# Performance work log

Measured on AMD Instinct MI355X. Metric: run time of the kernel, lower is better.

Reference implementation:

```python
import jax, jax.numpy as jnp
import numpy as np
from jax import lax

# NOTE: ResidualConvBlock and SS2DChanelFirst are reconstructed from the repo's
# conventions: ResidualConvBlock = act(conv3x3 -> act -> conv3x3 + 1x1 skip);
# SS2DChanelFirst = standard VMamba SS2D (in_proj -> dw-conv3x3 -> SiLU ->
# 4-direction cross-scan selective scan -> cross-merge -> LayerNorm -> *SiLU(z)
# gate -> out_proj) operating on NCHW tensors.

B, CIN, H, W = 4, 6, 64, 64
DM, DI, K, N, R, NL, GROUPS = 72, 144, 4, 8, 4, 2, 12


def conv2d(x, w, b=None, groups=1):
    out = lax.conv_general_dilated(x, w, (1, 1), 'SAME',
                                   dimension_numbers=('NCHW', 'OIHW', 'NCHW'),
                                   feature_group_count=groups)
    if b is not None:
        out = out + b[None, :, None, None]
    return out


def lrelu(x, s):
    return jnp.where(x >= 0, x, s * x)


def selective_scan(u, delta, A, Bs, Cs, D):
    # u, delta: (b,K,C,L); A: (K,C,N); Bs, Cs: (b,K,N,L); D: (K,C)
    b, k, c, l = u.shape
    n = A.shape[-1]
    ul = jnp.moveaxis(u, -1, 0)
    dl = jnp.moveaxis(delta, -1, 0)
    Bl = jnp.moveaxis(Bs, -1, 0)
    Cl = jnp.moveaxis(Cs, -1, 0)
    h0 = jnp.zeros((b, k, c, n), u.dtype)

    def step(h, xt):
        d_t, u_t, B_t, C_t = xt
        h = h * jnp.exp(d_t[..., None] * A) + (d_t * u_t)[..., None] * B_t[:, :, None, :]
        return h, jnp.einsum('bkcn,bkn->bkc', h, C_t)

    _, ys = lax.scan(step, h0, (dl, ul, Bl, Cl))
    return jnp.moveaxis(ys, 0, -1) + u * D[None, :, :, None]


def ss2d(x, in_w, dw_w, dw_b, xp_w, dtp_w, dtp_b, A_logs, Ds, ong, onb, op_w):
    b, dm, h_, w_ = x.shape
    l = h_ * w_
    xz = jnp.einsum('ec,bchw->behw', in_w, x)  # (b, 2*DI, h, w)
    xi, z = xz[:, :DI], xz[:, DI:]
    xi = jax.nn.silu(conv2d(xi, dw_w, dw_b, groups=DI))
    # cross-scan: row-major, col-major, and their reverses
    x0 = xi.reshape(b, DI, l)
    x1 = jnp.swapaxes(xi, 2, 3).reshape(b, DI, l)
    xs = jnp.stack([x0, x1, x0[..., ::-1], x1[..., ::-1]], axis=1)  # (b,4,DI,l)
    x_dbl = jnp.einsum('bkdl,kcd->bkcl', xs, xp_w)  # (b,4,R+2N,l)
    dts, Bs, Cs = x_dbl[:, :, :R], x_dbl[:, :, R:R + N], x_dbl[:, :, R + N:]
    dts = jnp.einsum('bkrl,kdr->bkdl', dts, dtp_w)
    delta = jax.nn.softplus(dts + dtp_b[None, :, :, None])
    A = -jnp.exp(A_logs).reshape(K, DI, N)
    ys = selective_scan(xs, delta, A, Bs, Cs, Ds.reshape(K, DI))  # (b,4,DI,l)
    # cross-merge
    y = ys[:, 0] + ys[:, 2, :, ::-1]
    yt = ys[:, 1] + ys[:, 3, :, ::-1]
    y = y + jnp.swapaxes(yt.reshape(b, DI, w_, h_), 2, 3).reshape(b, DI, l)
    y = jnp.swapaxes(y, 1, 2)  # (b,l,DI)
    mu = y.mean(-1, keepdims=True)
    var = ((y - mu) ** 2).mean(-1, keepdims=True)
    y = (y - mu) / jnp.sqrt(var + 1e-5) * ong + onb
    y = y * jax.nn.silu(jnp.swapaxes(z.reshape(b, DI, l), 1, 2))
    out = jnp.einsum('bld,ed->ble', y, op_w)  # (b,l,DM)
    return jnp.swapaxes(out, 1, 2).reshape(b, dm, h_, w_)


def groupnorm(x, g, bta, groups):
    b, c, h_, w_ = x.shape
    xg = x.reshape(b, groups, c // groups, h_ * w_)
    mu = xg.mean((2, 3), keepdims=True)
    var = ((xg - mu) ** 2).mean((2, 3), keepdims=True)
    xg = (xg - mu) / jnp.sqrt(var + 1e-5)
    return xg.reshape(b, c, h_, w_) * g[None, :, None, None] + bta[None, :, None, None]


def setup_inputs() -> dict:
    key = jax.random.key(0)
    ks = iter(jax.random.split(key, 32))
    nrm = lambda shp, s=0.05: jax.random.normal(next(ks), shp, jnp.float32) * s
    inp = {
        'image': jax.random.normal(next(ks), (B, CIN, H, W), jnp.float32),
        'cb_w1': nrm((DM, CIN, 3, 3), 0.1), 'cb_b1': nrm((DM,), 0.02),
        'cb_w2': nrm((DM, DM, 3, 3), 0.05), 'cb_b2': nrm((DM,), 0.02),
        'cb_ws': nrm((DM, CIN, 1, 1), 0.1), 'cb_bs': nrm((DM,), 0.02),
        'in_w': nrm((NL, 2 * DI, DM), 0.05),
        'dw_w': nrm((NL, DI, 1, 3, 3), 0.1), 'dw_b': nrm((NL, DI), 0.02),
        'xp_w': nrm((NL, K, R + 2 * N, DI), 0.05),
        'dtp_w': nrm((NL, K, DI, R), 0.1), 'dtp_b': nrm((NL, K, DI), 0.1),
        'A_logs': nrm((NL, K * DI, N), 0.5),
        'Ds': jnp.ones((NL, K * DI), jnp.float32) + nrm((NL, K * DI), 0.05),
        'ong': jnp.ones((NL, DI), jnp.float32), 'onb': jnp.zeros((NL, DI), jnp.float32),
        'op_w': nrm((NL, DM, DI), 0.05),
        'gn_g': jnp.ones((NL, DM), jnp.float32), 'gn_b': jnp.zeros((NL, DM), jnp.float32),
        'l1_w': nrm((NL, DM, DM), 0.1), 'l1_b': nrm((NL, DM), 0.02),
        'l2_w': nrm((NL, DM, DM), 0.1), 'l2_b': nrm((NL, DM), 0.02),
        'shrink_w': nrm((CIN, DM, 3, 3), 0.05), 'shrink_b': nrm((CIN,), 0.02),
    }
    return inp


def reference(image, cb_w1, cb_b1, cb_w2, cb_b2, cb_ws, cb_bs, in_w, dw_w, dw_b,
              xp_w, dtp_w, dtp_b, A_logs, Ds, ong, onb, op_w, gn_g, gn_b,
              l1_w, l1_b, l2_w, l2_b, shrink_w, shrink_b):
    # ResidualConvBlock (expand 6 -> 72), leaky_relu
    h = lrelu(conv2d(image, cb_w1, cb_b1), 0.01)
    h = conv2d(h, cb_w2, cb_b2) + conv2d(image, cb_ws, cb_bs)
    x = lrelu(h, 0.01)
    for i in range(NL):
        x = ss2d(x, in_w[i], dw_w[i], dw_b[i], xp_w[i], dtp_w[i], dtp_b[i],
                 A_logs[i], Ds[i], ong[i], onb[i], op_w[i])
        x = groupnorm(x, gn_g[i], gn_b[i], GROUPS)
        x = jnp.einsum('oc,bchw->bohw', l1_w[i], x) + l1_b[i][None, :, None, None]
        x = lrelu(x, 0.04)
        x = jnp.einsum('oc,bchw->bohw', l2_w[i], x) + l2_b[i][None, :, None, None]
    x = conv2d(x, shrink_w, shrink_b)
    return jax.nn.sigmoid(x)
```

## Files before the change

### kernel.cpp

```cpp
#include <hip/hip_runtime.h>
#include <math.h>

#define BB 4
#define CI 6
#define LL 4096
#define DMC 72
#define DIC 144
#define KD 4
#define NS 8
#define RD 4
#define NLAYER 2
#define GRP 12
#define NCH 128
#define TS 32
#define PP 4356

__device__ __forceinline__ float sigmoidf_(float x){ return 1.f/(1.f+__expf(-x)); }
__device__ __forceinline__ float siluf_(float x){ return x*sigmoidf_(x); }
__device__ __forceinline__ float softplusf_(float x){
  return fmaxf(x,0.f) + __logf(1.f + __expf(-fabsf(x)));
}

__device__ __forceinline__ int padidx(int p){ return 66*(p>>6) + (p&63) + 67; }

__device__ __forceinline__ int dirmap(int k, int l){
  switch(k & 3){
    case 0: return l;
    case 1: return ((l & 63) << 6) | (l >> 6);
    case 2: return (LL-1) - l;
    default: { int m = (LL-1) - l; return ((m & 63) << 6) | (m >> 6); }
  }
}

#define LOAD9(ip, a) do { \
  a[0]=(ip)[-67]; a[1]=(ip)[-66]; a[2]=(ip)[-65]; \
  a[3]=(ip)[-1];  a[4]=(ip)[0];   a[5]=(ip)[1];   \
  a[6]=(ip)[65];  a[7]=(ip)[66];  a[8]=(ip)[67];  } while(0)

__global__ void k_halo(float* __restrict__ pads, int nplanes){
  int plane = blockIdx.x;
  if (plane >= nplanes) return;
  int t = threadIdx.x;
  if (t >= 260) return;
  float* pl = pads + (size_t)plane*PP;
  int off;
  if (t < 132){
    int row = (t < 66) ? 0 : 65;
    int col = (t < 66) ? t : t-66;
    off = row*66 + col;
  } else {
    int j = t - 132;
    int col = (j < 64) ? 0 : 65;
    int row = 1 + (j & 63);
    off = row*66 + col;
  }
  pl[off] = 0.f;
}

__global__ void k_pad_img(const float* __restrict__ img, float* __restrict__ img_pad){
  int idx = blockIdx.x*256 + threadIdx.x;
  if (idx >= BB*CI*LL) return;
  int p = idx & 4095; int bc = idx >> 12;
  img_pad[(size_t)bc*PP + padidx(p)] = img[idx];
}

__global__ void k_conv1(const float* __restrict__ img_pad, const float* __restrict__ w,
                        const float* __restrict__ bias, float* __restrict__ tmp_pad){
  int bid = blockIdx.x;
  int t = bid & 15; int r = bid >> 4; int o = r % DMC; int b = r / DMC;
  int p = t*256 + threadIdx.x;
  int pb = padidx(p);
  float acc = bias[o];
  const float* wb = w + o*CI*9;
  #pragma unroll
  for (int ic=0; ic<CI; ++ic){
    const float* ip = img_pad + (size_t)(b*CI+ic)*PP + pb;
    float a[9]; LOAD9(ip, a);
    #pragma unroll
    for (int q=0;q<9;++q) acc += a[q]*wb[ic*9+q];
  }
  tmp_pad[(size_t)(b*DMC+o)*PP + pb] = acc >= 0.f ? acc : 0.01f*acc;
}

__global__ void k_conv2(const float* __restrict__ tmp_pad, const float* __restrict__ img,
                        const float* __restrict__ w2, const float* __restrict__ b2,
                        const float* __restrict__ wsc, const float* __restrict__ bsc,
                        float* __restrict__ xout){
  int bid = blockIdx.x;
  int t = bid & 15; int r = bid >> 4; int og = r % 18; int b = r / 18;
  int p = t*256 + threadIdx.x;
  int pb = padidx(p);
  float acc[4];
  #pragma unroll
  for (int j=0;j<4;++j) acc[j] = b2[og*4+j] + bsc[og*4+j];
  const float* ipb = tmp_pad + (size_t)b*DMC*PP + pb;
  const float* wb  = w2 + (size_t)(og*4)*DMC*9;
  #pragma unroll 2
  for (int ic=0; ic<DMC; ++ic){
    const float* ip = ipb + (size_t)ic*PP;
    float a[9]; LOAD9(ip, a);
    const float* wp = wb + ic*9;
    #pragma unroll
    for (int j=0;j<4;++j){
      float s = 0.f;
      #pragma unroll
      for (int q=0;q<9;++q) s += a[q]*wp[(size_t)j*DMC*9 + q];
      acc[j] += s;
    }
  }
  #pragma unroll
  for (int ic=0; ic<CI; ++ic){
    float v = img[((b*CI+ic)<<12)+p];
    #pragma unroll
    for (int j=0;j<4;++j) acc[j] += v * wsc[(og*4+j)*CI+ic];
  }
  #pragma unroll
  for (int j=0;j<4;++j){
    float a = acc[j];
    xout[((b*DMC+og*4+j)<<12)+p] = a >= 0.f ? a : 0.01f*a;
  }
}

__global__ void k_xz(const float* __restrict__ x, const float* __restrict__ inw,
                     float* __restrict__ xz_pad, float* __restrict__ z_t){
  int bid = blockIdx.x;
  int t = bid & 15; int r = bid >> 4; int eg = r % 36; int b = r / 36;
  int p = t*256 + threadIdx.x;
  float acc[8] = {0.f,0.f,0.f,0.f,0.f,0.f,0.f,0.f};
  for (int c0=0; c0<DMC; c0+=4){
    float a[4];
    #pragma unroll
    for (int q=0;q<4;++q) a[q] = x[((b*DMC+c0+q)<<12)+p];
    #pragma unroll
    for (int j=0;j<8;++j){
      float4 w = *(const float4*)(inw + (eg*8+j)*DMC + c0);
      acc[j] += a[0]*w.x + a[1]*w.y + a[2]*w.z + a[3]*w.w;
    }
  }
  if (eg < 18){
    int pb = padidx(p);
    #pragma unroll
    for (int j=0;j<8;++j) xz_pad[(size_t)(b*DIC+eg*8+j)*PP + pb] = acc[j];
  } else {
    float* zb = z_t + ((size_t)b*LL+p)*DIC + (eg*8-DIC);
    *(float4*)(zb)   = make_float4(acc[0],acc[1],acc[2],acc[3]);
    *(float4*)(zb+4) = make_float4(acc[4],acc[5],acc[6],acc[7]);
  }
}

__global__ void k_dw(const float* __restrict__ xz_pad, const float* __restrict__ dww,
                     const float* __restrict__ dwb, float* __restrict__ xi_t){
  int bid = blockIdx.x;
  int t = bid & 15; int r = bid >> 4; int c = r % DIC; int b = r / DIC;
  int p = t*256 + threadIdx.x;
  int pb = padidx(p);
  const float* ip = xz_pad + (size_t)(b*DIC+c)*PP + pb;
  const float* wp = dww + c*9;
  float a[9]; LOAD9(ip, a);
  float acc = dwb[c];
  #pragma unroll
  for (int q=0;q<9;++q) acc += a[q]*wp[q];
  xi_t[((size_t)b*LL+p)*DIC + c] = siluf_(acc);
}

__global__ void k_xdbl(const float* __restrict__ xi_t, const float* __restrict__ xpw,
                       float* __restrict__ xdbl){
  int bid = blockIdx.x;
  int t = bid & 15; int r = bid >> 4;
  int kk = r & 3; r >>= 2; int part = r & 3; int b = r >> 2;
  int p = t*256 + threadIdx.x;
  const float* xib = xi_t + ((size_t)b*LL + p)*DIC;
  const float* wk = xpw + (size_t)(kk*20 + part*5)*DIC;
  float acc[5] = {0.f,0.f,0.f,0.f,0.f};
  for (int d=0; d<DIC; d+=4){
    float4 v = *(const float4*)(xib + d);
    #pragma unroll
    for (int c=0;c<5;++c){
      float4 w = *(const float4*)(wk + (size_t)c*DIC + d);
      acc[c] += v.x*w.x + v.y*w.y + v.z*w.z + v.w*w.w;
    }
  }
  float* dst = xdbl + ((size_t)(b*KD+kk)*LL + p)*20 + part*5;
  #pragma unroll
  for (int c=0;c<5;++c) dst[c] = acc[c];
}

__device__ __forceinline__ void scan_decode(int idx, int& b, int& k, int& ch, int& c){
  c = idx % DIC;
  int r = idx / DIC;
  ch = r % NCH;
  r /= NCH;
  k = r & 3; b = r >> 2;
}

__global__ void k_p1(const float* __restrict__ xi_t, const float* __restrict__ xdbl,
                     const float* __restrict__ dtpw, const float* __restrict__ dtpb,
                     const float* __restrict__ alog,
                     float* __restrict__ cumA, float* __restrict__ hp){
  int idx = blockIdx.x*256 + threadIdx.x;
  if (idx >= BB*KD*NCH*DIC) return;
  int b,k,ch,c; scan_decode(idx,b,k,ch,c);
  float Arow[NS];
  #pragma unroll
  for (int n=0;n<NS;++n) Arow[n] = -__expf(alog[(k*DIC+c)*NS+n]);
  float4 wdt = *(const float4*)(dtpw + (k*DIC+c)*RD);
  float bdt = dtpb[k*DIC+c];
  const float* xd = xdbl + (size_t)(b*KD+k)*LL*20;
  const float* xib = xi_t + (size_t)b*LL*DIC + c;
  float h[NS];
  #pragma unroll
  for (int n=0;n<NS;++n) h[n]=0.f;
  float sumd = 0.f;
  #pragma unroll 2
  for (int t=0; t<TS; ++t){
    int l = ch*TS + t;
    int ps = dirmap(k,l);
    const float* row = xd + (size_t)ps*20;
    float4 q0 = *(const float4*)(row);
    float4 q1 = *(const float4*)(row+4);
    float4 q2 = *(const float4*)(row+8);
    float u = xib[(size_t)ps*DIC];
    float dt = bdt + q0.x*wdt.x + q0.y*wdt.y + q0.z*wdt.z + q0.w*wdt.w;
    dt = softplusf_(dt);
    sumd += dt;
    float du = dt*u;
    float Bv[NS] = {q1.x,q1.y,q1.z,q1.w,q2.x,q2.y,q2.z,q2.w};
    #pragma unroll
    for (int n=0;n<NS;++n)
      h[n] = h[n]*__expf(dt*Arow[n]) + du*Bv[n];
  }
  size_t base = ((size_t)((b*KD+k)*NCH + ch)*NS)*DIC + c;
  #pragma unroll
  for (int n=0;n<NS;++n) hp[base + n*DIC] = h[n];
  #pragma unroll
  for (int n=0;n<NS;++n) cumA[base + n*DIC] = __expf(sumd*Arow[n]);
}

__global__ void k_p2(const float* __restrict__ cumA, float* __restrict__ hp){
  int idx = blockIdx.x*256 + threadIdx.x;
  if (idx >= BB*KD*NS*DIC) return;
  int c = idx % DIC; int n = (idx/DIC) % NS; int bk = idx/(DIC*NS);
  float h = 0.f;
  #pragma unroll 4
  for (int ch=0; ch<NCH; ++ch){
    size_t base = ((size_t)(bk*NCH+ch)*NS + n)*DIC + c;
    float a = cumA[base];
    float pp = hp[base];
    hp[base] = h;
    h = a*h + pp;
  }
}

__global__ void k_p3(const float* __restrict__ xi_t, const float* __restrict__ xdbl,
                     const float* __restrict__ dtpw, const float* __restrict__ dtpb,
                     const float* __restrict__ alog, const float* __restrict__ Dsv,
                     const float* __restrict__ hin, float* __restrict__ y_t){
  int idx = blockIdx.x*256 + threadIdx.x;
  if (idx >= BB*KD*NCH*DIC) return;
  int b,k,ch,c; scan_decode(idx,b,k,ch,c);
  float Arow[NS];
  #pragma unroll
  for (int n=0;n<NS;++n) Arow[n] = -__expf(alog[(k*DIC+c)*NS+n]);
  float4 wdt = *(const float4*)(dtpw + (k*DIC+c)*RD);
  float bdt = dtpb[k*DIC+c];
  float Dv = Dsv[k*DIC+c];
  const float* xd = xdbl + (size_t)(b*KD+k)*LL*20;
  const float* xib = xi_t + (size_t)b*LL*DIC + c;
  float* yb = y_t + (size_t)b*LL*DIC + c;
  float h[NS];
  size_t base = ((size_t)((b*KD+k)*NCH + ch)*NS)*DIC + c;
  #pragma unroll
  for (int n=0;n<NS;++n) h[n] = hin[base + n*DIC];
  #pragma unroll 2
  for (int t=0; t<TS; ++t){
    int l = ch*TS + t;
    int ps = dirmap(k,l);
    const float* row = xd + (size_t)ps*20;
    float4 q0 = *(const float4*)(row);
    float4 q1 = *(const float4*)(row+4);
    float4 q2 = *(const float4*)(row+8);
    float4 q3 = *(const float4*)(row+12);
    float4 q4 = *(const float4*)(row+16);
    float u = xib[(size_t)ps*DIC];
    float dt = bdt + q0.x*wdt.x + q0.y*wdt.y + q0.z*wdt.z + q0.w*wdt.w;
    dt = softplusf_(dt);
    float du = dt*u;
    float Bv[NS] = {q1.x,q1.y,q1.z,q1.w,q2.x,q2.y,q2.z,q2.w};
    float Cv[NS] = {q3.x,q3.y,q3.z,q3.w,q4.x,q4.y,q4.z,q4.w};
    float y = 0.f;
    #pragma unroll
    for (int n=0;n<NS;++n){
      h[n] = h[n]*__expf(dt*Arow[n]) + du*Bv[n];
      y += h[n]*Cv[n];
    }
    y += u*Dv;
    atomicAdd(yb + (size_t)ps*DIC, y);
  }
}

__global__ void k_oproj(const float* __restrict__ y_t, const float* __restrict__ z_t,
                        const float* __restrict__ ong, const float* __restrict__ onb,
                        const float* __restrict__ opw, float* __restrict__ xout){
  __shared__ float ly[DIC*65];
  __shared__ float red1[4][64], red2[4][64];
  __shared__ float lmu[64], lrs[64];
  int bid = blockIdx.x;
  int tile = bid & 63; int b = bid >> 6;
  int pstart = tile*64;
  const float* src = y_t + ((size_t)b*LL + pstart)*DIC;
  for (int i = threadIdx.x; i < 64*DIC; i += 256){
    int px = i / DIC; int d = i - px*DIC;
    ly[d*65 + px] = src[i];
  }
  __syncthreads();
  int px = threadIdx.x & 63;
  int grp = threadIdx.x >> 6;
  {
    float s=0.f, q=0.f;
    for (int d=grp*36; d<grp*36+36; ++d){
      float v = ly[d*65+px]; s += v; q += v*v;
    }
    red1[grp][px]=s; red2[grp][px]=q;
  }
  __syncthreads();
  if (grp == 0){
    float st = red1[0][px]+red1[1][px]+red1[2][px]+red1[3][px];
    float qt = red2[0][px]+red2[1][px]+red2[2][px]+red2[3][px];
    float mu = st*(1.f/DIC);
    float var = qt*(1.f/DIC) - mu*mu;
    lmu[px] = mu;
    lrs[px] = rsqrtf(var + 1e-5f);
  }
  __syncthreads();
  const float* zsrc = z_t + ((size_t)b*LL + pstart)*DIC;
  for (int i = threadIdx.x; i < 64*DIC; i += 256){
    int ppx = i / DIC; int d = i - ppx*DIC;
    float zv = zsrc[i];
    float v = ly[d*65+ppx];
    ly[d*65+ppx] = ((v - lmu[ppx])*lrs[ppx]*ong[d] + onb[d]) * siluf_(zv);
  }
  __syncthreads();
  int ocg = __builtin_amdgcn_readfirstlane(grp);
  float acc[18];
  #pragma unroll
  for (int j=0;j<18;++j) acc[j]=0.f;
  const float* wb = opw + (size_t)ocg*18*DIC;
  #pragma unroll 4
  for (int d=0; d<DIC; ++d){
    float a = ly[d*65 + px];
    #pragma unroll
    for (int j=0;j<18;++j) acc[j] += a * wb[(size_t)j*DIC + d];
  }
  #pragma unroll
  for (int j=0;j<18;++j)
    xout[((size_t)(b*DMC + ocg*18 + j)<<12) + pstart + px] = acc[j];
}

__global__ void k_gn(float* __restrict__ x, const float* __restrict__ g,
                     const float* __restrict__ bta){
  __shared__ float s1[256], s2[256];
  int b = blockIdx.x / GRP; int gr = blockIdx.x % GRP;
  const int CG = DMC/GRP;
  float ls=0.f, lq=0.f;
  for (int i = threadIdx.x; i < CG*LL; i += 256){
    int c = gr*CG + (i>>12); int p = i & 4095;
    float v = x[((size_t)(b*DMC+c)<<12)+p];
    ls += v; lq += v*v;
  }
  s1[threadIdx.x]=ls; s2[threadIdx.x]=lq; __syncthreads();
  for (int s=128; s>0; s>>=1){
    if (threadIdx.x < s){ s1[threadIdx.x]+=s1[threadIdx.x+s]; s2[threadIdx.x]+=s2[threadIdx.x+s]; }
    __syncthreads();
  }
  float mu = s1[0]/(CG*LL);
  float var = s2[0]/(CG*LL) - mu*mu;
  float rs = rsqrtf(var + 1e-5f);
  for (int i = threadIdx.x; i < CG*LL; i += 256){
    int c = gr*CG + (i>>12); int p = i & 4095;
    size_t off = ((size_t)(b*DMC+c)<<12)+p;
    x[off] = (x[off]-mu)*rs*g[c] + bta[c];
  }
}

__global__ void k_dense(const float* __restrict__ xin, const float* __restrict__ w,
                        const float* __restrict__ bias, float* __restrict__ xout,
                        float* __restrict__ pad_out, int do_lrelu){
  int bid = blockIdx.x;
  int t = bid & 15; int r = bid >> 4; int eg = r % 18; int b = r / 18;
  int p = t*256 + threadIdx.x;
  float acc[4];
  #pragma unroll
  for (int j=0;j<4;++j) acc[j] = bias[eg*4+j];
  for (int c0=0; c0<DMC; c0+=4){
    float a[4];
    #pragma unroll
    for (int q=0;q<4;++q) a[q] = xin[((size_t)(b*DMC+c0+q)<<12)+p];
    #pragma unroll
    for (int j=0;j<4;++j){
      float4 w0 = *(const float4*)(w + (eg*4+j)*DMC + c0);
      acc[j] += a[0]*w0.x + a[1]*w0.y + a[2]*w0.z + a[3]*w0.w;
    }
  }
  int pb = padidx(p);
  #pragma unroll
  for (int j=0;j<4;++j){
    float a = acc[j];
    if (do_lrelu) a = a >= 0.f ? a : 0.04f*a;
    xout[((size_t)(b*DMC+eg*4+j)<<12)+p] = a;
    if (pad_out) pad_out[(size_t)(b*DMC+eg*4+j)*PP + pb] = a;
  }
}

__global__ void k_shrinkA(const float* __restrict__ x_pad, const float* __restrict__ w,
                          float* __restrict__ pacc){
  int bid = blockIdx.x;
  int t = bid & 15; int r = bid >> 4; int icg = r & 7; int b = r >> 3;
  int p = t*256 + threadIdx.x;
  int pb = padidx(p);
  float acc[6] = {0.f,0.f,0.f,0.f,0.f,0.f};
  const float* ipb = x_pad + (size_t)b*DMC*PP + pb;
  #pragma unroll
  for (int ii=0; ii<9; ++ii){
    int ic = icg*9 + ii;
    const float* ip = ipb + (size_t)ic*PP;
    float a[9]; LOAD9(ip, a);
    #pragma unroll
    for (int o=0;o<6;++o){
      const float* wp = w + (o*DMC+ic)*9;
      float s = 0.f;
      #pragma unroll
      for (int q=0;q<9;++q) s += a[q]*wp[q];
      acc[o] += s;
    }
  }
  #pragma unroll
  for (int o=0;o<6;++o)
    atomicAdd(pacc + ((size_t)(b*CI+o)<<12)+p, acc[o]);
}

__global__ void k_sig(const float* __restrict__ pacc, const float* __restrict__ bias,
                      float* __restrict__ out){
  int idx = blockIdx.x*256 + threadIdx.x;
  if (idx >= BB*CI*LL) return;
  int o = (idx>>12) % CI;
  out[idx] = sigmoidf_(pacc[idx] + bias[o]);
}

extern "C" void kernel_launch(void* const* d_in, const int* in_sizes, int n_in,
                              void* d_out, int out_size, void* d_ws, size_t ws_size,
                              hipStream_t stream){
  const float* image = (const float*)d_in[0];
  const float* cb_w1 = (const float*)d_in[1];
  const float* cb_b1 = (const float*)d_in[2];
  const float* cb_w2 = (const float*)d_in[3];
  const float* cb_b2 = (const float*)d_in[4];
  const float* cb_ws = (const float*)d_in[5];
  const float* cb_bs = (const float*)d_in[6];
  const float* in_w  = (const float*)d_in[7];
  const float* dw_w  = (const float*)d_in[8];
  const float* dw_b  = (const float*)d_in[9];
  const float* xp_w  = (const float*)d_in[10];
  const float* dtp_w = (const float*)d_in[11];
  const float* dtp_b = (const float*)d_in[12];
  const float* A_logs= (const float*)d_in[13];
  const float* Ds    = (const float*)d_in[14];
  const float* ong   = (const float*)d_in[15];
  const float* onb   = (const float*)d_in[16];
  const float* op_w  = (const float*)d_in[17];
  const float* gn_g  = (const float*)d_in[18];
  const float* gn_b  = (const float*)d_in[19];
  const float* l1_w  = (const float*)d_in[20];
  const float* l1_b  = (const float*)d_in[21];
  const float* l2_w  = (const float*)d_in[22];
  const float* l2_b  = (const float*)d_in[23];
  const float* sh_w  = (const float*)d_in[24];
  const float* sh_b  = (const float*)d_in[25];

  const size_t SZ_X  = (size_t)BB*DMC*LL;
  const size_t SZ_C  = (size_t)BB*DIC*LL;
  const size_t SZ_XD = (size_t)BB*KD*20*LL;
  const size_t SZ_IP = (size_t)BB*CI*PP;
  const size_t SZ_TP = (size_t)BB*DMC*PP;
  const size_t SZ_ZP = (size_t)BB*DIC*PP;

  float* ws = (float*)d_ws;
  size_t off = 0;
  float* x     = ws + off; off += SZ_X;
  float* tmp   = ws + off; off += SZ_X;
  float* z_t   = ws + off; off += SZ_C;
  float* xi_t  = ws + off; off += SZ_C;
  float* xdbl  = ws + off; off += SZ_XD;
  float* cumA  = ws + off; off += SZ_C;
  float* hp    = ws + off; off += SZ_C;
  float* pads  = ws + off;
  float* img_pad = pads;
  float* tmp_pad = img_pad + SZ_IP;
  float* xz_pad  = tmp_pad + SZ_TP;
  off += SZ_IP + SZ_TP + SZ_ZP;
  if (ws_size < off*sizeof(float)) return;
  float* y_t = cumA;

  dim3 blk(256);
  const int NPLANES = BB*CI + BB*DMC + BB*DIC;

  k_halo<<<dim3(NPLANES), blk, 0, stream>>>(pads, NPLANES);
  k_pad_img<<<dim3(BB*CI*16), blk, 0, stream>>>(image, img_pad);
  k_conv1<<<dim3(BB*DMC*16), blk, 0, stream>>>(img_pad, cb_w1, cb_b1, tmp_pad);
  k_conv2<<<dim3(BB*18*16), blk, 0, stream>>>(tmp_pad, image, cb_w2, cb_b2, cb_ws, cb_bs, x);

  for (int i=0; i<NLAYER; ++i){
    const float* in_w_i  = in_w  + (size_t)i*2*DIC*DMC;
    const float* dw_w_i  = dw_w  + (size_t)i*DIC*9;
    const float* dw_b_i  = dw_b  + (size_t)i*DIC;
    const float* xp_w_i  = xp_w  + (size_t)i*KD*20*DIC;
    const float* dtp_w_i = dtp_w + (size_t)i*KD*DIC*RD;
    const float* dtp_b_i = dtp_b + (size_t)i*KD*DIC;
    const float* alog_i  = A_logs+ (size_t)i*KD*DIC*NS;
    const float* Ds_i    = Ds    + (size_t)i*KD*DIC;
    const float* ong_i   = ong   + (size_t)i*DIC;
    const float* onb_i   = onb   + (size_t)i*DIC;
    const float* op_w_i  = op_w  + (size_t)i*DMC*DIC;
    const float* gn_g_i  = gn_g  + (size_t)i*DMC;
    const float* gn_b_i  = gn_b  + (size_t)i*DMC;
    const float* l1_w_i  = l1_w  + (size_t)i*DMC*DMC;
    const float* l1_b_i  = l1_b  + (size_t)i*DMC;
    const float* l2_w_i  = l2_w  + (size_t)i*DMC*DMC;
    const float* l2_b_i  = l2_b  + (size_t)i*DMC;

    k_xz  <<<dim3(BB*36*16), blk, 0, stream>>>(x, in_w_i, xz_pad, z_t);
    k_dw  <<<dim3(BB*DIC*16), blk, 0, stream>>>(xz_pad, dw_w_i, dw_b_i, xi_t);
    k_xdbl<<<dim3(BB*KD*KD*16), blk, 0, stream>>>(xi_t, xp_w_i, xdbl);
    k_p1  <<<dim3(BB*KD*NCH*DIC/256), blk, 0, stream>>>(xi_t, xdbl, dtp_w_i, dtp_b_i, alog_i, cumA, hp);
    k_p2  <<<dim3(BB*KD*NS*DIC/256), blk, 0, stream>>>(cumA, hp);
    hipMemsetAsync(y_t, 0, SZ_C*sizeof(float), stream);
    k_p3  <<<dim3(BB*KD*NCH*DIC/256), blk, 0, stream>>>(xi_t, xdbl, dtp_w_i, dtp_b_i, alog_i, Ds_i, hp, y_t);
    k_oproj<<<dim3(BB*64), blk, 0, stream>>>(y_t, z_t, ong_i, onb_i, op_w_i, x);
    k_gn  <<<dim3(BB*GRP), blk, 0, stream>>>(x, gn_g_i, gn_b_i);
    k_dense<<<dim3(BB*18*16), blk, 0, stream>>>(x, l1_w_i, l1_b_i, tmp, (float*)nullptr, 1);
    k_dense<<<dim3(BB*18*16), blk, 0, stream>>>(tmp, l2_w_i, l2_b_i, x,
                                                (i==NLAYER-1) ? tmp_pad : (float*)nullptr, 0);
  }

  hipMemsetAsync(tmp, 0, (size_t)BB*CI*LL*sizeof(float), stream);
  k_shrinkA<<<dim3(BB*8*16), blk, 0, stream>>>(tmp_pad, sh_w, tmp);
  k_sig<<<dim3((BB*CI*LL+255)/256), blk, 0, stream>>>(tmp, sh_b, (float*)d_out);
}
```

Before: 528.2 us.

## Split kernels for more parallelism, parallelize groupnorm, and use exp2 in scan

Splits conv2 across two input-channel halves and accumulates with atomics, after a separate init kernel writes the skip path and bias. The leaky ReLU moves into the first in-projection load. Groupnorm becomes a parallel stats pass plus a per-channel scale/shift that is folded into the first dense layer, and the second dense layer applies the previous leaky ReLU on load. xdbl, dense and shrink kernels get finer output splits, oproj uses 512 threads, and the scan uses exp2f with a pre-scaled A. The goal is higher occupancy on small grids, removing the serialized 48-block groupnorm and cheaper exponentials, at the cost of extra launches and atomic traffic.

```diff
diff --git a/kernel.cpp b/kernel.cpp
--- a/kernel.cpp
+++ b/kernel.cpp
@@ -14,6 +14,7 @@
 #define NCH 128
 #define TS 32
 #define PP 4356
+#define L2E 1.4426950408889634f
 
 __device__ __forceinline__ float sigmoidf_(float x){ return 1.f/(1.f+__expf(-x)); }
 __device__ __forceinline__ float siluf_(float x){ return x*sigmoidf_(x); }
@@ -82,21 +83,39 @@
   tmp_pad[(size_t)(b*DMC+o)*PP + pb] = acc >= 0.f ? acc : 0.01f*acc;
 }
 
-__global__ void k_conv2(const float* __restrict__ tmp_pad, const float* __restrict__ img,
-                        const float* __restrict__ w2, const float* __restrict__ b2,
-                        const float* __restrict__ wsc, const float* __restrict__ bsc,
-                        float* __restrict__ xout){
+__global__ void k_conv2init(const float* __restrict__ img, const float* __restrict__ b2,
+                            const float* __restrict__ wsc, const float* __restrict__ bsc,
+                            float* __restrict__ xout){
   int bid = blockIdx.x;
   int t = bid & 15; int r = bid >> 4; int og = r % 18; int b = r / 18;
   int p = t*256 + threadIdx.x;
+  float acc[4];
+  #pragma unroll
+  for (int j=0;j<4;++j) acc[j] = b2[og*4+j] + bsc[og*4+j];
+  #pragma unroll
+  for (int ic=0; ic<CI; ++ic){
+    float v = img[((b*CI+ic)<<12)+p];
+    #pragma unroll
+    for (int j=0;j<4;++j) acc[j] += v * wsc[(og*4+j)*CI+ic];
+  }
+  #pragma unroll
+  for (int j=0;j<4;++j)
+    xout[((b*DMC+og*4+j)<<12)+p] = acc[j];
+}
+
+__global__ void k_conv2(const float* __restrict__ tmp_pad,
+                        const float* __restrict__ w2, float* __restrict__ xout){
+  int bid = blockIdx.x;
+  int t = bid & 15; int r = bid >> 4; int og = r % 18; r /= 18;
+  int icg = r & 1; int b = r >> 1;
+  int p = t*256 + threadIdx.x;
   int pb = padidx(p);
-  float acc[4];
-  #pragma unroll
-  for (int j=0;j<4;++j) acc[j] = b2[og*4+j] + bsc[og*4+j];
+  float acc[4] = {0.f,0.f,0.f,0.f};
   const float* ipb = tmp_pad + (size_t)b*DMC*PP + pb;
   const float* wb  = w2 + (size_t)(og*4)*DMC*9;
   #pragma unroll 2
-  for (int ic=0; ic<DMC; ++ic){
+  for (int ii=0; ii<36; ++ii){
+    int ic = icg*36 + ii;
     const float* ip = ipb + (size_t)ic*PP;
     float a[9]; LOAD9(ip, a);
     const float* wp = wb + ic*9;
@@ -109,20 +128,12 @@
     }
   }
   #pragma unroll
-  for (int ic=0; ic<CI; ++ic){
-    float v = img[((b*CI+ic)<<12)+p];
-    #pragma unroll
-    for (int j=0;j<4;++j) acc[j] += v * wsc[(og*4+j)*CI+ic];
-  }
-  #pragma unroll
-  for (int j=0;j<4;++j){
-    float a = acc[j];
-    xout[((b*DMC+og*4+j)<<12)+p] = a >= 0.f ? a : 0.01f*a;
-  }
+  for (int j=0;j<4;++j)
+    atomicAdd(xout + ((b*DMC+og*4+j)<<12)+p, acc[j]);
 }
 
 __global__ void k_xz(const float* __restrict__ x, const float* __restrict__ inw,
-                     float* __restrict__ xz_pad, float* __restrict__ z_t){
+                     float* __restrict__ xz_pad, float* __restrict__ z_t, int relu){
   int bid = blockIdx.x;
   int t = bid & 15; int r = bid >> 4; int eg = r % 36; int b = r / 36;
   int p = t*256 + threadIdx.x;
@@ -131,6 +142,10 @@
     float a[4];
     #pragma unroll
     for (int q=0;q<4;++q) a[q] = x[((b*DMC+c0+q)<<12)+p];
+    if (relu){
+      #pragma unroll
+      for (int q=0;q<4;++q) a[q] = a[q] >= 0.f ? a[q] : 0.01f*a[q];
+    }
     #pragma unroll
     for (int j=0;j<8;++j){
       float4 w = *(const float4*)(inw + (eg*8+j)*DMC + c0);
@@ -167,22 +182,21 @@
                        float* __restrict__ xdbl){
   int bid = blockIdx.x;
   int t = bid & 15; int r = bid >> 4;
-  int kk = r & 3; r >>= 2; int part = r & 3; int b = r >> 2;
+  int kk = r & 3; r >>= 2; int part = r % 10; int b = r / 10;
   int p = t*256 + threadIdx.x;
   const float* xib = xi_t + ((size_t)b*LL + p)*DIC;
-  const float* wk = xpw + (size_t)(kk*20 + part*5)*DIC;
-  float acc[5] = {0.f,0.f,0.f,0.f,0.f};
+  const float* wk = xpw + (size_t)(kk*20 + part*2)*DIC;
+  float acc[2] = {0.f,0.f};
   for (int d=0; d<DIC; d+=4){
     float4 v = *(const float4*)(xib + d);
     #pragma unroll
-    for (int c=0;c<5;++c){
+    for (int c=0;c<2;++c){
       float4 w = *(const float4*)(wk + (size_t)c*DIC + d);
       acc[c] += v.x*w.x + v.y*w.y + v.z*w.z + v.w*w.w;
     }
   }
-  float* dst = xdbl + ((size_t)(b*KD+kk)*LL + p)*20 + part*5;
-  #pragma unroll
-  for (int c=0;c<5;++c) dst[c] = acc[c];
+  float* dst = xdbl + ((size_t)(b*KD+kk)*LL + p)*20 + part*2;
+  dst[0] = acc[0]; dst[1] = acc[1];
 }
 
 __device__ __forceinline__ void scan_decode(int idx, int& b, int& k, int& ch, int& c){
@@ -202,7 +216,7 @@
   int b,k,ch,c; scan_decode(idx,b,k,ch,c);
   float Arow[NS];
   #pragma unroll
-  for (int n=0;n<NS;++n) Arow[n] = -__expf(alog[(k*DIC+c)*NS+n]);
+  for (int n=0;n<NS;++n) Arow[n] = -__expf(alog[(k*DIC+c)*NS+n]) * L2E;
   float4 wdt = *(const float4*)(dtpw + (k*DIC+c)*RD);
   float bdt = dtpb[k*DIC+c];
   const float* xd = xdbl + (size_t)(b*KD+k)*LL*20;
@@ -227,13 +241,13 @@
     float Bv[NS] = {q1.x,q1.y,q1.z,q1.w,q2.x,q2.y,q2.z,q2.w};
     #pragma unroll
     for (int n=0;n<NS;++n)
-      h[n] = h[n]*__expf(dt*Arow[n]) + du*Bv[n];
+      h[n] = h[n]*exp2f(dt*Arow[n]) + du*Bv[n];
   }
   size_t base = ((size_t)((b*KD+k)*NCH + ch)*NS)*DIC + c;
   #pragma unroll
   for (int n=0;n<NS;++n) hp[base + n*DIC] = h[n];
   #pragma unroll
-  for (int n=0;n<NS;++n) cumA[base + n*DIC] = __expf(sumd*Arow[n]);
+  for (int n=0;n<NS;++n) cumA[base + n*DIC] = exp2f(sumd*Arow[n]);
 }
 
 __global__ void k_p2(const float* __restrict__ cumA, float* __restrict__ hp){
@@ -260,7 +274,7 @@
   int b,k,ch,c; scan_decode(idx,b,k,ch,c);
   float Arow[NS];
   #pragma unroll
-  for (int n=0;n<NS;++n) Arow[n] = -__expf(alog[(k*DIC+c)*NS+n]);
+  for (int n=0;n<NS;++n) Arow[n] = -__expf(alog[(k*DIC+c)*NS+n]) * L2E;
   float4 wdt = *(const float4*)(dtpw + (k*DIC+c)*RD);
   float bdt = dtpb[k*DIC+c];
   float Dv = Dsv[k*DIC+c];
@@ -290,7 +304,7 @@
     float y = 0.f;
     #pragma unroll
     for (int n=0;n<NS;++n){
-      h[n] = h[n]*__expf(dt*Arow[n]) + du*Bv[n];
+      h[n] = h[n]*exp2f(dt*Arow[n]) + du*Bv[n];
       y += h[n]*Cv[n];
     }
     y += u*Dv;
@@ -302,13 +316,13 @@
                         const float* __restrict__ ong, const float* __restrict__ onb,
                         const float* __restrict__ opw, float* __restrict__ xout){
   __shared__ float ly[DIC*65];
-  __shared__ float red1[4][64], red2[4][64];
+  __shared__ float red1[8][64], red2[8][64];
   __shared__ float lmu[64], lrs[64];
   int bid = blockIdx.x;
   int tile = bid & 63; int b = bid >> 6;
   int pstart = tile*64;
   const float* src = y_t + ((size_t)b*LL + pstart)*DIC;
-  for (int i = threadIdx.x; i < 64*DIC; i += 256){
+  for (int i = threadIdx.x; i < 64*DIC; i += 512){
     int px = i / DIC; int d = i - px*DIC;
     ly[d*65 + px] = src[i];
   }
@@ -317,15 +331,16 @@
   int grp = threadIdx.x >> 6;
   {
     float s=0.f, q=0.f;
-    for (int d=grp*36; d<grp*36+36; ++d){
+    for (int d=grp*18; d<grp*18+18; ++d){
       float v = ly[d*65+px]; s += v; q += v*v;
     }
     red1[grp][px]=s; red2[grp][px]=q;
   }
   __syncthreads();
   if (grp == 0){
-    float st = red1[0][px]+red1[1][px]+red1[2][px]+red1[3][px];
-    float qt = red2[0][px]+red2[1][px]+red2[2][px]+red2[3][px];
+    float st=0.f, qt=0.f;
+    #pragma unroll
+    for (int g=0;g<8;++g){ st += red1[g][px]; qt += red2[g][px]; }
     float mu = st*(1.f/DIC);
     float var = qt*(1.f/DIC) - mu*mu;
     lmu[px] = mu;
@@ -333,7 +348,7 @@
   }
   __syncthreads();
   const float* zsrc = z_t + ((size_t)b*LL + pstart)*DIC;
-  for (int i = threadIdx.x; i < 64*DIC; i += 256){
+  for (int i = threadIdx.x; i < 64*DIC; i += 512){
     int ppx = i / DIC; int d = i - ppx*DIC;
     float zv = zsrc[i];
     float v = ly[d*65+ppx];
@@ -341,29 +356,30 @@
   }
   __syncthreads();
   int ocg = __builtin_amdgcn_readfirstlane(grp);
-  float acc[18];
-  #pragma unroll
-  for (int j=0;j<18;++j) acc[j]=0.f;
-  const float* wb = opw + (size_t)ocg*18*DIC;
+  float acc[9];
+  #pragma unroll
+  for (int j=0;j<9;++j) acc[j]=0.f;
+  const float* wb = opw + (size_t)ocg*9*DIC;
   #pragma unroll 4
   for (int d=0; d<DIC; ++d){
     float a = ly[d*65 + px];
     #pragma unroll
-    for (int j=0;j<18;++j) acc[j] += a * wb[(size_t)j*DIC + d];
-  }
-  #pragma unroll
-  for (int j=0;j<18;++j)
-    xout[((size_t)(b*DMC + ocg*18 + j)<<12) + pstart + px] = acc[j];
-}
-
-__global__ void k_gn(float* __restrict__ x, const float* __restrict__ g,
-                     const float* __restrict__ bta){
+    for (int j=0;j<9;++j) acc[j] += a * wb[(size_t)j*DIC + d];
+  }
+  #pragma unroll
+  for (int j=0;j<9;++j)
+    xout[((size_t)(b*DMC + ocg*9 + j)<<12) + pstart + px] = acc[j];
+}
+
+__global__ void k_gnA(const float* __restrict__ x, float* __restrict__ stats){
   __shared__ float s1[256], s2[256];
-  int b = blockIdx.x / GRP; int gr = blockIdx.x % GRP;
-  const int CG = DMC/GRP;
+  int bid = blockIdx.x;
+  int t = bid & 15; int r = bid >> 4; int gr = r % GRP; int b = r / GRP;
   float ls=0.f, lq=0.f;
-  for (int i = threadIdx.x; i < CG*LL; i += 256){
-    int c = gr*CG + (i>>12); int p = i & 4095;
+  #pragma unroll
+  for (int it=0; it<6; ++it){
+    int i = t*1536 + it*256 + threadIdx.x;
+    int c = gr*6 + (i>>12); int p = i & 4095;
     float v = x[((size_t)(b*DMC+c)<<12)+p];
     ls += v; lq += v*v;
   }
@@ -372,56 +388,93 @@
     if (threadIdx.x < s){ s1[threadIdx.x]+=s1[threadIdx.x+s]; s2[threadIdx.x]+=s2[threadIdx.x+s]; }
     __syncthreads();
   }
-  float mu = s1[0]/(CG*LL);
-  float var = s2[0]/(CG*LL) - mu*mu;
+  if (threadIdx.x == 0){
+    atomicAdd(stats + (b*GRP+gr)*2,     s1[0]);
+    atomicAdd(stats + (b*GRP+gr)*2 + 1, s2[0]);
+  }
+}
+
+__global__ void k_gnAB(const float* __restrict__ stats, const float* __restrict__ g,
+                       const float* __restrict__ bta, float* __restrict__ gnab){
+  int idx = blockIdx.x*256 + threadIdx.x;
+  if (idx >= BB*DMC) return;
+  int c = idx % DMC; int b = idx / DMC; int gr = c / 6;
+  float s = stats[(b*GRP+gr)*2];
+  float q = stats[(b*GRP+gr)*2 + 1];
+  const float inv = 1.f/(6.f*LL);
+  float mu = s*inv;
+  float var = q*inv - mu*mu;
   float rs = rsqrtf(var + 1e-5f);
-  for (int i = threadIdx.x; i < CG*LL; i += 256){
-    int c = gr*CG + (i>>12); int p = i & 4095;
-    size_t off = ((size_t)(b*DMC+c)<<12)+p;
-    x[off] = (x[off]-mu)*rs*g[c] + bta[c];
-  }
-}
-
-__global__ void k_dense(const float* __restrict__ xin, const float* __restrict__ w,
-                        const float* __restrict__ bias, float* __restrict__ xout,
-                        float* __restrict__ pad_out, int do_lrelu){
-  int bid = blockIdx.x;
-  int t = bid & 15; int r = bid >> 4; int eg = r % 18; int b = r / 18;
-  int p = t*256 + threadIdx.x;
-  float acc[4];
-  #pragma unroll
-  for (int j=0;j<4;++j) acc[j] = bias[eg*4+j];
+  float A = rs*g[c];
+  gnab[idx] = A;
+  gnab[BB*DMC + idx] = bta[c] - mu*A;
+}
+
+__global__ void k_dense1(const float* __restrict__ xin, const float* __restrict__ gnab,
+                         const float* __restrict__ w, const float* __restrict__ bias,
+                         float* __restrict__ xout){
+  int bid = blockIdx.x;
+  int t = bid & 15; int r = bid >> 4; int eg = r % 36; int b = r / 36;
+  int p = t*256 + threadIdx.x;
+  float acc[2] = { bias[eg*2], bias[eg*2+1] };
+  const float* Aab = gnab + b*DMC;
+  const float* Bab = gnab + BB*DMC + b*DMC;
   for (int c0=0; c0<DMC; c0+=4){
     float a[4];
     #pragma unroll
-    for (int q=0;q<4;++q) a[q] = xin[((size_t)(b*DMC+c0+q)<<12)+p];
-    #pragma unroll
-    for (int j=0;j<4;++j){
-      float4 w0 = *(const float4*)(w + (eg*4+j)*DMC + c0);
+    for (int q=0;q<4;++q){
+      float v = xin[((size_t)(b*DMC+c0+q)<<12)+p];
+      a[q] = v*Aab[c0+q] + Bab[c0+q];
+    }
+    #pragma unroll
+    for (int j=0;j<2;++j){
+      float4 w0 = *(const float4*)(w + (eg*2+j)*DMC + c0);
       acc[j] += a[0]*w0.x + a[1]*w0.y + a[2]*w0.z + a[3]*w0.w;
     }
   }
-  int pb = padidx(p);
-  #pragma unroll
-  for (int j=0;j<4;++j){
-    float a = acc[j];
-    if (do_lrelu) a = a >= 0.f ? a : 0.04f*a;
-    xout[((size_t)(b*DMC+eg*4+j)<<12)+p] = a;
-    if (pad_out) pad_out[(size_t)(b*DMC+eg*4+j)*PP + pb] = a;
+  #pragma unroll
+  for (int j=0;j<2;++j)
+    xout[((size_t)(b*DMC+eg*2+j)<<12)+p] = acc[j];
+}
+
+__global__ void k_dense2(const float* __restrict__ xin, const float* __restrict__ w,
+                         const float* __restrict__ bias, float* __restrict__ xout,
+                         float* __restrict__ pad_out){
+  int bid = blockIdx.x;
+  int t = bid & 15; int r = bid >> 4; int eg = r % 36; int b = r / 36;
+  int p = t*256 + threadIdx.x;
+  float acc[2] = { bias[eg*2], bias[eg*2+1] };
+  for (int c0=0; c0<DMC; c0+=4){
+    float a[4];
+    #pragma unroll
+    for (int q=0;q<4;++q){
+      float v = xin[((size_t)(b*DMC+c0+q)<<12)+p];
+      a[q] = v >= 0.f ? v : 0.04f*v;
+    }
+    #pragma unroll
+    for (int j=0;j<2;++j){
+      float4 w0 = *(const float4*)(w + (eg*2+j)*DMC + c0);
+      acc[j] += a[0]*w0.x + a[1]*w0.y + a[2]*w0.z + a[3]*w0.w;
+    }
+  }
+  #pragma unroll
+  for (int j=0;j<2;++j){
+    xout[((size_t)(b*DMC+eg*2+j)<<12)+p] = acc[j];
+    if (pad_out) pad_out[(size_t)(b*DMC+eg*2+j)*PP + padidx(p)] = acc[j];
   }
 }
 
 __global__ void k_shrinkA(const float* __restrict__ x_pad, const float* __restrict__ w,
                           float* __restrict__ pacc){
   int bid = blockIdx.x;
-  int t = bid & 15; int r = bid >> 4; int icg = r & 7; int b = r >> 3;
+  int t = bid & 15; int r = bid >> 4; int icg = r % 24; int b = r / 24;
   int p = t*256 + threadIdx.x;
   int pb = padidx(p);
   float acc[6] = {0.f,0.f,0.f,0.f,0.f,0.f};
   const float* ipb = x_pad + (size_t)b*DMC*PP + pb;
   #pragma unroll
-  for (int ii=0; ii<9; ++ii){
-    int ic = icg*9 + ii;
+  for (int ii=0; ii<3; ++ii){
+    int ic = icg*3 + ii;
     const float* ip = ipb + (size_t)ic*PP;
     float a[9]; LOAD9(ip, a);
     #pragma unroll
@@ -497,6 +550,8 @@
   float* tmp_pad = img_pad + SZ_IP;
   float* xz_pad  = tmp_pad + SZ_TP;
   off += SZ_IP + SZ_TP + SZ_ZP;
+  float* gnstats = ws + off; off += 2*BB*GRP;
+  float* gnab    = ws + off; off += 2*BB*DMC;
   if (ws_size < off*sizeof(float)) return;
   float* y_t = cumA;
 
@@ -506,7 +561,8 @@
   k_halo<<<dim3(NPLANES), blk, 0, stream>>>(pads, NPLANES);
   k_pad_img<<<dim3(BB*CI*16), blk, 0, stream>>>(image, img_pad);
   k_conv1<<<dim3(BB*DMC*16), blk, 0, stream>>>(img_pad, cb_w1, cb_b1, tmp_pad);
-  k_conv2<<<dim3(BB*18*16), blk, 0, stream>>>(tmp_pad, image, cb_w2, cb_b2, cb_ws, cb_bs, x);
+  k_conv2init<<<dim3(BB*18*16), blk, 0, stream>>>(image, cb_b2, cb_ws, cb_bs, x);
+  k_conv2<<<dim3(BB*2*18*16), blk, 0, stream>>>(tmp_pad, cb_w2, x);
 
   for (int i=0; i<NLAYER; ++i){
     const float* in_w_i  = in_w  + (size_t)i*2*DIC*DMC;
@@ -527,21 +583,23 @@
     const float* l2_w_i  = l2_w  + (size_t)i*DMC*DMC;
     const float* l2_b_i  = l2_b  + (size_t)i*DMC;
 
-    k_xz  <<<dim3(BB*36*16), blk, 0, stream>>>(x, in_w_i, xz_pad, z_t);
+    k_xz  <<<dim3(BB*36*16), blk, 0, stream>>>(x, in_w_i, xz_pad, z_t, (i==0)?1:0);
     k_dw  <<<dim3(BB*DIC*16), blk, 0, stream>>>(xz_pad, dw_w_i, dw_b_i, xi_t);
-    k_xdbl<<<dim3(BB*KD*KD*16), blk, 0, stream>>>(xi_t, xp_w_i, xdbl);
+    k_xdbl<<<dim3(BB*10*KD*16), blk, 0, stream>>>(xi_t, xp_w_i, xdbl);
     k_p1  <<<dim3(BB*KD*NCH*DIC/256), blk, 0, stream>>>(xi_t, xdbl, dtp_w_i, dtp_b_i, alog_i, cumA, hp);
     k_p2  <<<dim3(BB*KD*NS*DIC/256), blk, 0, stream>>>(cumA, hp);
     hipMemsetAsync(y_t, 0, SZ_C*sizeof(float), stream);
     k_p3  <<<dim3(BB*KD*NCH*DIC/256), blk, 0, stream>>>(xi_t, xdbl, dtp_w_i, dtp_b_i, alog_i, Ds_i, hp, y_t);
-    k_oproj<<<dim3(BB*64), blk, 0, stream>>>(y_t, z_t, ong_i, onb_i, op_w_i, x);
-    k_gn  <<<dim3(BB*GRP), blk, 0, stream>>>(x, gn_g_i, gn_b_i);
-    k_dense<<<dim3(BB*18*16), blk, 0, stream>>>(x, l1_w_i, l1_b_i, tmp, (float*)nullptr, 1);
-    k_dense<<<dim3(BB*18*16), blk, 0, stream>>>(tmp, l2_w_i, l2_b_i, x,
-                                                (i==NLAYER-1) ? tmp_pad : (float*)nullptr, 0);
+    k_oproj<<<dim3(BB*64), dim3(512), 0, stream>>>(y_t, z_t, ong_i, onb_i, op_w_i, x);
+    hipMemsetAsync(gnstats, 0, 2*BB*GRP*sizeof(float), stream);
+    k_gnA <<<dim3(BB*GRP*16), blk, 0, stream>>>(x, gnstats);
+    k_gnAB<<<dim3(2), blk, 0, stream>>>(gnstats, gn_g_i, gn_b_i, gnab);
+    k_dense1<<<dim3(BB*36*16), blk, 0, stream>>>(x, gnab, l1_w_i, l1_b_i, tmp);
+    k_dense2<<<dim3(BB*36*16), blk, 0, stream>>>(tmp, l2_w_i, l2_b_i, x,
+                                                 (i==NLAYER-1) ? tmp_pad : (float*)nullptr);
   }
 
   hipMemsetAsync(tmp, 0, (size_t)BB*CI*LL*sizeof(float), stream);
-  k_shrinkA<<<dim3(BB*8*16), blk, 0, stream>>>(tmp_pad, sh_w, tmp);
+  k_shrinkA<<<dim3(BB*24*16), blk, 0, stream>>>(tmp_pad, sh_w, tmp);
   k_sig<<<dim3((BB*CI*LL+255)/256), blk, 0, stream>>>(tmp, sh_b, (float*)d_out);
 }
```

Result: slower. 538.8 us (+2.0%).
